# Performance work log

Measured on AMD Instinct MI355X. Metric: run time of the kernel, lower is better.

The kernel has to match this reference:

```python
import jax, jax.numpy as jnp
import numpy as np

N, K, D, VOCAB = 20000, 32, 128, 100000
NEG = -1e30  # finite large-negative so all-masked rows don't produce NaN softmax


def setup_inputs() -> dict:
    key = jax.random.key(0)
    ks = jax.random.split(key, 10)
    return {
        "nodes": jax.random.randint(ks[0], (N,), 0, VOCAB),
        "neigh_idx": jax.random.randint(ks[1], (N, K), 0, VOCAB),
        "neigh_len": jax.random.randint(ks[2], (N,), 0, K + 1),
        "u2e": jax.random.normal(ks[3], (VOCAB, D), dtype=jnp.float32),
        "W1": jax.random.normal(ks[4], (D, 2 * D), dtype=jnp.float32) * 0.05,
        "b1": jax.random.normal(ks[5], (D,), dtype=jnp.float32) * 0.05,
        "W2": jax.random.normal(ks[6], (D, D), dtype=jnp.float32) * 0.05,
        "b2": jax.random.normal(ks[7], (D,), dtype=jnp.float32) * 0.05,
        "W3": jax.random.normal(ks[8], (1, D), dtype=jnp.float32) * 0.05,
        "b3": jax.random.normal(ks[9], (1,), dtype=jnp.float32) * 0.05,
    }


def reference(nodes, neigh_idx, neigh_len, u2e, W1, b1, W2, b2, W3, b3):
    # self features: [N, D]
    self_feats = u2e[nodes]
    # neighbor features gather: [N, K, D]
    e_u = u2e[neigh_idx]
    # GraphRec Attention: cat(neighbor, self-broadcast) -> MLP -> softmax over K
    x = jnp.concatenate(
        [e_u, jnp.broadcast_to(self_feats[:, None, :], e_u.shape)], axis=-1
    )  # [N, K, 2D]
    h = jax.nn.relu(jnp.einsum("nkf,df->nkd", x, W1) + b1)
    h = jax.nn.relu(jnp.einsum("nkd,ed->nke", h, W2) + b2)
    logits = jnp.einsum("nkd,od->nko", h, W3)[..., 0] + b3[0]  # [N, K]
    mask = jnp.arange(K)[None, :] < neigh_len[:, None]  # [N, K]
    att = jax.nn.softmax(jnp.where(mask, logits, NEG), axis=1)
    att = jnp.where(mask, att, 0.0)  # zero out padded slots (and all-empty rows)
    # attention-weighted neighbor aggregation: [N, D]
    agg = jnp.einsum("nk,nkd->nd", att, e_u)
    has_neigh = (neigh_len > 0)[:, None]
    return jnp.where(has_neigh, (agg + self_feats) * 0.5, self_feats)
```

## Files before the change

### kernel.cpp

```cpp
#include <hip/hip_runtime.h>
#include <hip/hip_bf16.h>
#include <stdint.h>

#define KN 32
#define D  128
#define NNODES 20000
#define GRID 2500

typedef __bf16 bf16;
typedef __bf16 bf16x8 __attribute__((ext_vector_type(8)));
typedef float  f32x4  __attribute__((ext_vector_type(4)));

#define X_STRIDE  136
#define H_STRIDE  136
#define EU_STRIDE 132

__global__ __launch_bounds__(256) void pack_weights_kernel(
    const float* __restrict__ W1, const float* __restrict__ W2,
    bf16* __restrict__ w1p, bf16* __restrict__ w2p)
{
    int t = blockIdx.x * 256 + threadIdx.x;
    if (t < 32768) {
        int j = t & 7, lane = (t >> 3) & 63, kt = (t >> 9) & 7, nt = t >> 12;
        int d = nt * 16 + (lane & 15);
        int f = kt * 32 + ((lane >> 4) << 3) + j;
        w1p[t] = (bf16)W1[d * 256 + f];
    } else if (t < 49152) {
        int u = t - 32768;
        int j = u & 7, lane = (u >> 3) & 63, kt = (u >> 9) & 3, nt = u >> 11;
        int e  = nt * 16 + (lane & 15);
        int dd = kt * 32 + ((lane >> 4) << 3) + j;
        w2p[u] = (bf16)W2[e * 128 + dd];
    }
}

__global__ __launch_bounds__(256, 3) void graphrec_agg_kernel(
    const int*   __restrict__ nodes,
    const int*   __restrict__ neigh_idx,
    const int*   __restrict__ neigh_len,
    const float* __restrict__ u2e,
    const float* __restrict__ b1,
    const float* __restrict__ b2,
    const float* __restrict__ W3,
    const float* __restrict__ b3,
    const bf16*  __restrict__ w1p,
    const bf16*  __restrict__ w2p,
    float*       __restrict__ out)
{
    __shared__ alignas(16) bf16  x_bf[KN * X_STRIDE];
    __shared__ alignas(16) bf16  h1_bf[KN * H_STRIDE];
    __shared__ alignas(16) float eu_f[KN * EU_STRIDE];
    __shared__ alignas(16) float self_f[D];
    __shared__ alignas(16) bf16  self_bf[D];
    __shared__ float lpart[4 * KN];
    __shared__ float att_s[KN];

    const int t    = threadIdx.x;
    const int lane = t & 63;
    const int wave = t >> 6;
    const int ln15 = lane & 15;
    const int quad = lane >> 4;
    const int nt0  = wave * 2;

    const float bias1_0 = b1[nt0 * 16 + ln15];
    const float bias1_1 = b1[(nt0 + 1) * 16 + ln15];
    const float bias2_0 = b2[nt0 * 16 + ln15];
    const float bias2_1 = b2[(nt0 + 1) * 16 + ln15];
    const float w3_0    = W3[nt0 * 16 + ln15];
    const float w3_1    = W3[(nt0 + 1) * 16 + ln15];
    const float b3v     = b3[0];

    bf16x8 w1r[2][8];
    #pragma unroll
    for (int nt = 0; nt < 2; ++nt)
        #pragma unroll
        for (int ft = 0; ft < 8; ++ft)
            w1r[nt][ft] = *(const bf16x8*)(w1p + ((nt0 + nt) * 8 + ft) * 512 + lane * 8);
    bf16x8 w2r[2][4];
    #pragma unroll
    for (int nt = 0; nt < 2; ++nt)
        #pragma unroll
        for (int kt = 0; kt < 4; ++kt)
            w2r[nt][kt] = *(const bf16x8*)(w2p + ((nt0 + nt) * 4 + kt) * 512 + lane * 8);

    for (int n = blockIdx.x; n < NNODES; n += GRID) {
        const int len = neigh_len[n];

        {
            int k  = t >> 3;
            int f0 = (t & 7) << 4;
            int idx = neigh_idx[n * KN + k];
            const float* src = u2e + (size_t)idx * D + f0;
            float4 a0 = *(const float4*)(src);
            float4 a1 = *(const float4*)(src + 4);
            float4 a2 = *(const float4*)(src + 8);
            float4 a3 = *(const float4*)(src + 12);
            float* df = eu_f + k * EU_STRIDE + f0;
            *(float4*)(df)      = a0; *(float4*)(df + 4)  = a1;
            *(float4*)(df + 8)  = a2; *(float4*)(df + 12) = a3;
            float vr[16];
            *(float4*)(vr)      = a0; *(float4*)(vr + 4)  = a1;
            *(float4*)(vr + 8)  = a2; *(float4*)(vr + 12) = a3;
            bf16x8 v0, v1;
            #pragma unroll
            for (int i = 0; i < 8; ++i) { v0[i] = (bf16)vr[i]; v1[i] = (bf16)vr[8 + i]; }
            *(bf16x8*)(x_bf + k * X_STRIDE + f0)     = v0;
            *(bf16x8*)(x_bf + k * X_STRIDE + f0 + 8) = v1;
        }
        if (t < D) {
            float s = u2e[(size_t)nodes[n] * D + t];
            self_f[t]  = s;
            self_bf[t] = (bf16)s;
        }
        __syncthreads();

        bf16x8 sa[4];
        #pragma unroll
        for (int i = 0; i < 4; ++i)
            sa[i] = *(const bf16x8*)(self_bf + i * 32 + quad * 8);

        f32x4 c00 = {0.f,0.f,0.f,0.f}, c01 = c00, c10 = c00, c11 = c00;
        #pragma unroll
        for (int ft = 0; ft < 4; ++ft) {
            bf16x8 a0 = *(const bf16x8*)(x_bf + ln15 * X_STRIDE + ft * 32 + quad * 8);
            bf16x8 a1 = *(const bf16x8*)(x_bf + (16 + ln15) * X_STRIDE + ft * 32 + quad * 8);
            c00 = __builtin_amdgcn_mfma_f32_16x16x32_bf16(a0, w1r[0][ft], c00, 0, 0, 0);
            c01 = __builtin_amdgcn_mfma_f32_16x16x32_bf16(a0, w1r[1][ft], c01, 0, 0, 0);
            c10 = __builtin_amdgcn_mfma_f32_16x16x32_bf16(a1, w1r[0][ft], c10, 0, 0, 0);
            c11 = __builtin_amdgcn_mfma_f32_16x16x32_bf16(a1, w1r[1][ft], c11, 0, 0, 0);
        }
        #pragma unroll
        for (int ft = 4; ft < 8; ++ft) {
            bf16x8 a = sa[ft - 4];
            c00 = __builtin_amdgcn_mfma_f32_16x16x32_bf16(a, w1r[0][ft], c00, 0, 0, 0);
            c01 = __builtin_amdgcn_mfma_f32_16x16x32_bf16(a, w1r[1][ft], c01, 0, 0, 0);
            c10 = __builtin_amdgcn_mfma_f32_16x16x32_bf16(a, w1r[0][ft], c10, 0, 0, 0);
            c11 = __builtin_amdgcn_mfma_f32_16x16x32_bf16(a, w1r[1][ft], c11, 0, 0, 0);
        }
        {
            #pragma unroll
            for (int r = 0; r < 4; ++r) {
                int row = quad * 4 + r;
                h1_bf[row * H_STRIDE + nt0 * 16 + ln15]              = (bf16)fmaxf(c00[r] + bias1_0, 0.f);
                h1_bf[row * H_STRIDE + (nt0 + 1) * 16 + ln15]        = (bf16)fmaxf(c01[r] + bias1_1, 0.f);
                h1_bf[(16 + row) * H_STRIDE + nt0 * 16 + ln15]       = (bf16)fmaxf(c10[r] + bias1_0, 0.f);
                h1_bf[(16 + row) * H_STRIDE + (nt0 + 1) * 16 + ln15] = (bf16)fmaxf(c11[r] + bias1_1, 0.f);
            }
        }
        __syncthreads();

        f32x4 d00 = {0.f,0.f,0.f,0.f}, d01 = d00, d10 = d00, d11 = d00;
        #pragma unroll
        for (int kt = 0; kt < 4; ++kt) {
            bf16x8 a0 = *(const bf16x8*)(h1_bf + ln15 * H_STRIDE + kt * 32 + quad * 8);
            bf16x8 a1 = *(const bf16x8*)(h1_bf + (16 + ln15) * H_STRIDE + kt * 32 + quad * 8);
            d00 = __builtin_amdgcn_mfma_f32_16x16x32_bf16(a0, w2r[0][kt], d00, 0, 0, 0);
            d01 = __builtin_amdgcn_mfma_f32_16x16x32_bf16(a0, w2r[1][kt], d01, 0, 0, 0);
            d10 = __builtin_amdgcn_mfma_f32_16x16x32_bf16(a1, w2r[0][kt], d10, 0, 0, 0);
            d11 = __builtin_amdgcn_mfma_f32_16x16x32_bf16(a1, w2r[1][kt], d11, 0, 0, 0);
        }
        {
            #pragma unroll
            for (int r = 0; r < 4; ++r) {
                float p0 = w3_0 * fmaxf(d00[r] + bias2_0, 0.f)
                         + w3_1 * fmaxf(d01[r] + bias2_1, 0.f);
                float p1 = w3_0 * fmaxf(d10[r] + bias2_0, 0.f)
                         + w3_1 * fmaxf(d11[r] + bias2_1, 0.f);
                #pragma unroll
                for (int o = 1; o < 16; o <<= 1) {
                    p0 += __shfl_xor(p0, o);
                    p1 += __shfl_xor(p1, o);
                }
                if (ln15 == 0) {
                    lpart[wave * KN + quad * 4 + r]      = p0;
                    lpart[wave * KN + 16 + quad * 4 + r] = p1;
                }
            }
        }
        __syncthreads();

        if (t < 64) {
            int k = t & 31;
            float lg = lpart[k] + lpart[KN + k] + lpart[2 * KN + k] + lpart[3 * KN + k] + b3v;
            bool act = (t < 32) && (k < len);
            float l = act ? lg : -1e30f;
            float m = l;
            #pragma unroll
            for (int o = 1; o < 32; o <<= 1) m = fmaxf(m, __shfl_xor(m, o));
            float e = act ? expf(l - m) : 0.f;
            float s = e;
            #pragma unroll
            for (int o = 1; o < 32; o <<= 1) s += __shfl_xor(s, o);
            if (t < 32) att_s[k] = (s > 0.f) ? (e / s) : 0.f;
        }
        __syncthreads();

        if (t < D) {
            float a = 0.f;
            #pragma unroll
            for (int k = 0; k < KN; ++k) a += att_s[k] * eu_f[k * EU_STRIDE + t];
            float sf = self_f[t];
            out[(size_t)n * D + t] = (len > 0) ? 0.5f * (a + sf) : sf;
        }
        __syncthreads();
    }
}

extern "C" void kernel_launch(void* const* d_in, const int* in_sizes, int n_in,
                              void* d_out, int out_size, void* d_ws, size_t ws_size,
                              hipStream_t stream) {
    const int*   nodes     = (const int*)d_in[0];
    const int*   neigh_idx = (const int*)d_in[1];
    const int*   neigh_len = (const int*)d_in[2];
    const float* u2e       = (const float*)d_in[3];
    const float* W1        = (const float*)d_in[4];
    const float* b1        = (const float*)d_in[5];
    const float* W2        = (const float*)d_in[6];
    const float* b2        = (const float*)d_in[7];
    const float* W3        = (const float*)d_in[8];
    const float* b3        = (const float*)d_in[9];
    float* out = (float*)d_out;

    bf16* w1p = (bf16*)d_ws;
    bf16* w2p = w1p + 32768;

    pack_weights_kernel<<<192, 256, 0, stream>>>(W1, W2, w1p, w2p);
    graphrec_agg_kernel<<<GRID, 256, 0, stream>>>(nodes, neigh_idx, neigh_len, u2e,
                                                  b1, b2, W3, b3, w1p, w2p, out);
}
```

Measured before the change: 235.3 us.

## Gather embeddings directly into LDS and process two nodes per iteration

Embedding rows are now loaded straight from global memory into LDS with global_load_lds, replacing the register round-trip and the separate bf16 copy. The bf16 conversion now happens when MFMA operands are read from LDS. Each block handles two nodes per iteration and runs a fixed four iterations, so the indices for the next pair are prefetched into registers while the current pair's loads are in flight. This cuts register traffic and barriers per node, but uses more LDS per block, which may lower occupancy. It also hardcodes the grid-times-eight-nodes coverage, and the lenA/lenB reads and the pidx overwrite ordering look fragile.

```diff
diff --git a/kernel.cpp b/kernel.cpp
--- a/kernel.cpp
+++ b/kernel.cpp
@@ -6,14 +6,21 @@
 #define D  128
 #define NNODES 20000
 #define GRID 2500
+#define ITERS 4
 
 typedef __bf16 bf16;
 typedef __bf16 bf16x8 __attribute__((ext_vector_type(8)));
 typedef float  f32x4  __attribute__((ext_vector_type(4)));
 
-#define X_STRIDE  136
-#define H_STRIDE  136
-#define EU_STRIDE 132
+#define CHUNK_DW 260
+#define EU_NODE_DW (16 * CHUNK_DW)
+#define H_STRIDE 136
+
+#define GL2LDS(src, dst) __builtin_amdgcn_global_load_lds(                 \
+    (const __attribute__((address_space(1))) void*)(src),                  \
+    (__attribute__((address_space(3))) void*)(dst), 16, 0, 0)
+
+#define MFMA(a, b, c) __builtin_amdgcn_mfma_f32_16x16x32_bf16((a), (b), (c), 0, 0, 0)
 
 __global__ __launch_bounds__(256) void pack_weights_kernel(
     const float* __restrict__ W1, const float* __restrict__ W2,
@@ -47,14 +54,12 @@
     const bf16*  __restrict__ w2p,
     float*       __restrict__ out)
 {
-    __shared__ alignas(16) bf16  x_bf[KN * X_STRIDE];
-    __shared__ alignas(16) bf16  h1_bf[KN * H_STRIDE];
-    __shared__ alignas(16) float eu_f[KN * EU_STRIDE];
-    __shared__ alignas(16) float self_f[D];
-    __shared__ alignas(16) bf16  self_bf[D];
-    __shared__ float lpart[4 * KN];
-    __shared__ float att_s[KN];
-
+    __shared__ alignas(16) float eu[2 * EU_NODE_DW];
+    __shared__ alignas(16) bf16  h1[2 * KN * H_STRIDE];
+    __shared__ alignas(16) float self_f[2 * D];
+    __shared__ float lpart[2][4 * KN];
+    __shared__ float att_s[2][KN];
+    __shared__ int   pidx[68];
     const int t    = threadIdx.x;
     const int lane = t & 63;
     const int wave = t >> 6;
@@ -83,83 +88,122 @@
         for (int kt = 0; kt < 4; ++kt)
             w2r[nt][kt] = *(const bf16x8*)(w2p + ((nt0 + nt) * 4 + kt) * 512 + lane * 8);
 
-    for (int n = blockIdx.x; n < NNODES; n += GRID) {
-        const int len = neigh_len[n];
+    if (t < 68) {
+        int a = blockIdx.x * 8;
+        const int* base; int off;
+        if (t < 64)      { base = neigh_idx; off = (a + (t >> 5)) * KN + (t & 31); }
+        else if (t < 66) { base = nodes;     off = a + (t & 1); }
+        else             { base = neigh_len; off = a + (t & 1); }
+        pidx[t] = base[off];
+    }
+    __syncthreads();
+
+    for (int it = 0; it < ITERS; ++it) {
+        const int nA   = blockIdx.x * 8 + it * 2;
+        const int lenA = pidx[66];
+        const int lenB = pidx[67];
 
         {
-            int k  = t >> 3;
-            int f0 = (t & 7) << 4;
-            int idx = neigh_idx[n * KN + k];
-            const float* src = u2e + (size_t)idx * D + f0;
-            float4 a0 = *(const float4*)(src);
-            float4 a1 = *(const float4*)(src + 4);
-            float4 a2 = *(const float4*)(src + 8);
-            float4 a3 = *(const float4*)(src + 12);
-            float* df = eu_f + k * EU_STRIDE + f0;
-            *(float4*)(df)      = a0; *(float4*)(df + 4)  = a1;
-            *(float4*)(df + 8)  = a2; *(float4*)(df + 12) = a3;
-            float vr[16];
-            *(float4*)(vr)      = a0; *(float4*)(vr + 4)  = a1;
-            *(float4*)(vr + 8)  = a2; *(float4*)(vr + 12) = a3;
-            bf16x8 v0, v1;
-            #pragma unroll
-            for (int i = 0; i < 8; ++i) { v0[i] = (bf16)vr[i]; v1[i] = (bf16)vr[8 + i]; }
-            *(bf16x8*)(x_bf + k * X_STRIDE + f0)     = v0;
-            *(bf16x8*)(x_bf + k * X_STRIDE + f0 + 8) = v1;
-        }
-        if (t < D) {
-            float s = u2e[(size_t)nodes[n] * D + t];
-            self_f[t]  = s;
-            self_bf[t] = (bf16)s;
-        }
-        __syncthreads();
-
-        bf16x8 sa[4];
-        #pragma unroll
-        for (int i = 0; i < 4; ++i)
-            sa[i] = *(const bf16x8*)(self_bf + i * 32 + quad * 8);
-
-        f32x4 c00 = {0.f,0.f,0.f,0.f}, c01 = c00, c10 = c00, c11 = c00;
-        #pragma unroll
-        for (int ft = 0; ft < 4; ++ft) {
-            bf16x8 a0 = *(const bf16x8*)(x_bf + ln15 * X_STRIDE + ft * 32 + quad * 8);
-            bf16x8 a1 = *(const bf16x8*)(x_bf + (16 + ln15) * X_STRIDE + ft * 32 + quad * 8);
-            c00 = __builtin_amdgcn_mfma_f32_16x16x32_bf16(a0, w1r[0][ft], c00, 0, 0, 0);
-            c01 = __builtin_amdgcn_mfma_f32_16x16x32_bf16(a0, w1r[1][ft], c01, 0, 0, 0);
-            c10 = __builtin_amdgcn_mfma_f32_16x16x32_bf16(a1, w1r[0][ft], c10, 0, 0, 0);
-            c11 = __builtin_amdgcn_mfma_f32_16x16x32_bf16(a1, w1r[1][ft], c11, 0, 0, 0);
-        }
-        #pragma unroll
-        for (int ft = 4; ft < 8; ++ft) {
-            bf16x8 a = sa[ft - 4];
-            c00 = __builtin_amdgcn_mfma_f32_16x16x32_bf16(a, w1r[0][ft], c00, 0, 0, 0);
-            c01 = __builtin_amdgcn_mfma_f32_16x16x32_bf16(a, w1r[1][ft], c01, 0, 0, 0);
-            c10 = __builtin_amdgcn_mfma_f32_16x16x32_bf16(a, w1r[0][ft], c10, 0, 0, 0);
-            c11 = __builtin_amdgcn_mfma_f32_16x16x32_bf16(a, w1r[1][ft], c11, 0, 0, 0);
-        }
+            const int half = lane >> 5;
+            const int colb = (lane & 31) << 4;
+            #pragma unroll
+            for (int nd = 0; nd < 2; ++nd) {
+                #pragma unroll
+                for (int j = 0; j < 4; ++j) {
+                    int chunk = wave * 4 + j;
+                    int idx   = pidx[nd * KN + chunk + (half << 4)];
+                    const char* src = (const char*)(u2e + (size_t)idx * D) + colb;
+                    GL2LDS(src, eu + nd * EU_NODE_DW + chunk * CHUNK_DW);
+                }
+            }
+            if (wave == 0) {
+                int sidx = pidx[64 + half];
+                const char* src = (const char*)(u2e + (size_t)sidx * D) + colb;
+                GL2LDS(src, self_f);
+            }
+        }
+        int pf = 0;
         {
+            int a = blockIdx.x * 8 + (((it + 1) & 3) << 1);
+            if (t < 68) {
+                const int* base; int off;
+                if (t < 64)      { base = neigh_idx; off = (a + (t >> 5)) * KN + (t & 31); }
+                else if (t < 66) { base = nodes;     off = a + (t & 1); }
+                else             { base = neigh_len; off = a + (t & 1); }
+                pf = base[off];
+            }
+        }
+        __syncthreads();
+        if (t < 68) pidx[t] = pf;
+
+        #pragma unroll
+        for (int nd = 0; nd < 2; ++nd) {
+            const float* euN = eu + nd * EU_NODE_DW;
+            const float* sfN = self_f + nd * D;
+            bf16* h1N = h1 + nd * KN * H_STRIDE;
+
+            bf16x8 sa[4];
+            #pragma unroll
+            for (int i = 0; i < 4; ++i) {
+                f32x4 u0 = *(const f32x4*)(sfN + i * 32 + quad * 8);
+                f32x4 u1 = *(const f32x4*)(sfN + i * 32 + quad * 8 + 4);
+                bf16x8 a;
+                #pragma unroll
+                for (int e = 0; e < 4; ++e) { a[e] = (bf16)u0[e]; a[4 + e] = (bf16)u1[e]; }
+                sa[i] = a;
+            }
+            f32x4 c00 = {0.f,0.f,0.f,0.f}, c01 = c00, c10 = c00, c11 = c00;
+            const int r0 = ln15 * CHUNK_DW;
+            #pragma unroll
+            for (int ft = 0; ft < 4; ++ft) {
+                int off = ft * 32 + quad * 8;
+                f32x4 u0 = *(const f32x4*)(euN + r0 + off);
+                f32x4 u1 = *(const f32x4*)(euN + r0 + off + 4);
+                f32x4 v0 = *(const f32x4*)(euN + r0 + 128 + off);
+                f32x4 v1 = *(const f32x4*)(euN + r0 + 128 + off + 4);
+                bf16x8 a0, a1;
+                #pragma unroll
+                for (int e = 0; e < 4; ++e) {
+                    a0[e] = (bf16)u0[e]; a0[4 + e] = (bf16)u1[e];
+                    a1[e] = (bf16)v0[e]; a1[4 + e] = (bf16)v1[e];
+                }
+                c00 = MFMA(a0, w1r[0][ft], c00);
+                c01 = MFMA(a0, w1r[1][ft], c01);
+                c10 = MFMA(a1, w1r[0][ft], c10);
+                c11 = MFMA(a1, w1r[1][ft], c11);
+            }
+            #pragma unroll
+            for (int ft = 4; ft < 8; ++ft) {
+                bf16x8 a = sa[ft - 4];
+                c00 = MFMA(a, w1r[0][ft], c00);
+                c01 = MFMA(a, w1r[1][ft], c01);
+                c10 = MFMA(a, w1r[0][ft], c10);
+                c11 = MFMA(a, w1r[1][ft], c11);
+            }
             #pragma unroll
             for (int r = 0; r < 4; ++r) {
                 int row = quad * 4 + r;
-                h1_bf[row * H_STRIDE + nt0 * 16 + ln15]              = (bf16)fmaxf(c00[r] + bias1_0, 0.f);
-                h1_bf[row * H_STRIDE + (nt0 + 1) * 16 + ln15]        = (bf16)fmaxf(c01[r] + bias1_1, 0.f);
-                h1_bf[(16 + row) * H_STRIDE + nt0 * 16 + ln15]       = (bf16)fmaxf(c10[r] + bias1_0, 0.f);
-                h1_bf[(16 + row) * H_STRIDE + (nt0 + 1) * 16 + ln15] = (bf16)fmaxf(c11[r] + bias1_1, 0.f);
-            }
-        }
-        __syncthreads();
-
-        f32x4 d00 = {0.f,0.f,0.f,0.f}, d01 = d00, d10 = d00, d11 = d00;
-        #pragma unroll
-        for (int kt = 0; kt < 4; ++kt) {
-            bf16x8 a0 = *(const bf16x8*)(h1_bf + ln15 * H_STRIDE + kt * 32 + quad * 8);
-            bf16x8 a1 = *(const bf16x8*)(h1_bf + (16 + ln15) * H_STRIDE + kt * 32 + quad * 8);
-            d00 = __builtin_amdgcn_mfma_f32_16x16x32_bf16(a0, w2r[0][kt], d00, 0, 0, 0);
-            d01 = __builtin_amdgcn_mfma_f32_16x16x32_bf16(a0, w2r[1][kt], d01, 0, 0, 0);
-            d10 = __builtin_amdgcn_mfma_f32_16x16x32_bf16(a1, w2r[0][kt], d10, 0, 0, 0);
-            d11 = __builtin_amdgcn_mfma_f32_16x16x32_bf16(a1, w2r[1][kt], d11, 0, 0, 0);
-        }
-        {
+                h1N[row * H_STRIDE + nt0 * 16 + ln15]              = (bf16)fmaxf(c00[r] + bias1_0, 0.f);
+                h1N[row * H_STRIDE + (nt0 + 1) * 16 + ln15]        = (bf16)fmaxf(c01[r] + bias1_1, 0.f);
+                h1N[(16 + row) * H_STRIDE + nt0 * 16 + ln15]       = (bf16)fmaxf(c10[r] + bias1_0, 0.f);
+                h1N[(16 + row) * H_STRIDE + (nt0 + 1) * 16 + ln15] = (bf16)fmaxf(c11[r] + bias1_1, 0.f);
+            }
+        }
+        __syncthreads();
+
+        #pragma unroll
+        for (int nd = 0; nd < 2; ++nd) {
+            const bf16* h1N = h1 + nd * KN * H_STRIDE;
+            f32x4 d00 = {0.f,0.f,0.f,0.f}, d01 = d00, d10 = d00, d11 = d00;
+            #pragma unroll
+            for (int kt = 0; kt < 4; ++kt) {
+                bf16x8 a0 = *(const bf16x8*)(h1N + ln15 * H_STRIDE + kt * 32 + quad * 8);
+                bf16x8 a1 = *(const bf16x8*)(h1N + (16 + ln15) * H_STRIDE + kt * 32 + quad * 8);
+                d00 = MFMA(a0, w2r[0][kt], d00);
+                d01 = MFMA(a0, w2r[1][kt], d01);
+                d10 = MFMA(a1, w2r[0][kt], d10);
+                d11 = MFMA(a1, w2r[1][kt], d11);
+            }
             #pragma unroll
             for (int r = 0; r < 4; ++r) {
                 float p0 = w3_0 * fmaxf(d00[r] + bias2_0, 0.f)
@@ -172,17 +216,19 @@
                     p1 += __shfl_xor(p1, o);
                 }
                 if (ln15 == 0) {
-                    lpart[wave * KN + quad * 4 + r]      = p0;
-                    lpart[wave * KN + 16 + quad * 4 + r] = p1;
-                }
-            }
-        }
-        __syncthreads();
-
-        if (t < 64) {
-            int k = t & 31;
-            float lg = lpart[k] + lpart[KN + k] + lpart[2 * KN + k] + lpart[3 * KN + k] + b3v;
-            bool act = (t < 32) && (k < len);
+                    lpart[nd][wave * KN + quad * 4 + r]      = p0;
+                    lpart[nd][wave * KN + 16 + quad * 4 + r] = p1;
+                }
+            }
+        }
+        __syncthreads();
+
+        if (wave < 2) {
+            int nd = wave, k = lane & 31;
+            float lg = lpart[nd][k] + lpart[nd][KN + k] + lpart[nd][2 * KN + k]
+                     + lpart[nd][3 * KN + k] + b3v;
+            int len = nd ? lenB : lenA;
+            bool act = (lane < 32) && (k < len);
             float l = act ? lg : -1e30f;
             float m = l;
             #pragma unroll
@@ -191,16 +237,20 @@
             float s = e;
             #pragma unroll
             for (int o = 1; o < 32; o <<= 1) s += __shfl_xor(s, o);
-            if (t < 32) att_s[k] = (s > 0.f) ? (e / s) : 0.f;
-        }
-        __syncthreads();
-
-        if (t < D) {
-            float a = 0.f;
-            #pragma unroll
-            for (int k = 0; k < KN; ++k) a += att_s[k] * eu_f[k * EU_STRIDE + t];
-            float sf = self_f[t];
-            out[(size_t)n * D + t] = (len > 0) ? 0.5f * (a + sf) : sf;
+            if (lane < 32) att_s[nd][k] = (s > 0.f) ? (e / s) : 0.f;
+        }
+        __syncthreads();
+
+        {
+            int nd = t >> 7, d = t & 127;
+            const float* euN = eu + nd * EU_NODE_DW;
+            float acc = 0.f;
+            #pragma unroll
+            for (int k = 0; k < KN; ++k)
+                acc += att_s[nd][k] * euN[(k & 15) * CHUNK_DW + ((k >> 4) << 7) + d];
+            float sf = self_f[nd * D + d];
+            int len = nd ? lenB : lenA;
+            out[(size_t)(nA + nd) * D + d] = (len > 0) ? 0.5f * (acc + sf) : sf;
         }
         __syncthreads();
     }
```

New measurement: 326.5 us. 1.39x slower.
